# Kernel optimization log

Measured on AMD Instinct MI355X. Metric: run time of the kernel, lower is better.

Reference implementation:

```python
import jax, jax.numpy as jnp
import numpy as np

H = 2048      # hidden_size
K = 1024      # bottleneck_size
R = 3         # number of roles
B = 8         # batch
S = 2048      # sequence length
LN_EPS = 1e-5


def setup_inputs() -> dict:
    key = jax.random.key(0)
    ks = jax.random.split(key, 8)
    # torch nn.Linear default init ~ U(-1/sqrt(fan_in), 1/sqrt(fan_in)); scale similarly
    sd_d = 1.0 / np.sqrt(H)
    sd_u = 1.0 / np.sqrt(K)
    return {
        "role": jax.random.randint(ks[0], (B,), 0, R),
        "hidden_states": jax.random.normal(ks[1], (B, S, H), dtype=jnp.float32),
        # stacked per-role adapter params
        "W_down": jax.random.uniform(ks[2], (R, H, K), jnp.float32, -sd_d, sd_d),
        "b_down": jax.random.uniform(ks[3], (R, K), jnp.float32, -sd_d, sd_d),
        "W_up": jax.random.uniform(ks[4], (R, K, H), jnp.float32, -sd_u, sd_u),
        "b_up": jax.random.uniform(ks[5], (R, H), jnp.float32, -sd_u, sd_u),
        "gamma": jnp.ones((R, H), jnp.float32),
        "beta": jnp.zeros((R, H), jnp.float32),
    }


def reference(role, hidden_states, W_down, b_down, W_up, b_up, gamma, beta):
    # gather per-sample adapter params by role id: [B, H, K] etc.
    h = jnp.einsum("bsh,bhk->bsk", hidden_states, W_down[role]) + b_down[role][:, None, :]
    h = jax.nn.gelu(h, approximate=False)  # torch nn.GELU default = exact erf
    u = jnp.einsum("bsk,bkh->bsh", h, W_up[role]) + b_up[role][:, None, :]
    y = hidden_states + u
    # LayerNorm over last dim
    mean = jnp.mean(y, axis=-1, keepdims=True)
    var = jnp.mean(jnp.square(y - mean), axis=-1, keepdims=True)
    yn = (y - mean) * jax.lax.rsqrt(var + LN_EPS)
    return yn * gamma[role][:, None, :] + beta[role][:, None, :]
```

## Files before the change

### kernel.cpp

```cpp
#include <hip/hip_runtime.h>
#include <hip/hip_bf16.h>

#define H 2048
#define K 1024
#define R 3
#define BB 8
#define S 2048

typedef __bf16 bf16x8 __attribute__((ext_vector_type(8)));
typedef float f32x4 __attribute__((ext_vector_type(4)));
typedef unsigned short ushort8 __attribute__((ext_vector_type(8)));

static __device__ __forceinline__ unsigned short f2bf(float f) {
    unsigned int u = __float_as_uint(f);
    u += 0x7FFFu + ((u >> 16) & 1u);
    return (unsigned short)(u >> 16);
}

#define GLOAD_LDS16(g, l)                                                      \
    __builtin_amdgcn_global_load_lds(                                          \
        (const __attribute__((address_space(1))) void*)(g),                    \
        (__attribute__((address_space(3))) void*)(l), 16, 0, 0)

__global__ __launch_bounds__(256) void cvt_hs(const float* __restrict__ in,
                                              unsigned short* __restrict__ out,
                                              int n8) {
    int stride = gridDim.x * blockDim.x;
    for (int i = blockIdx.x * blockDim.x + threadIdx.x; i < n8; i += stride) {
        const float4* p = (const float4*)(in + (size_t)i * 8);
        float4 a = p[0], b = p[1];
        union { unsigned short us[8]; ushort8 v; } o;
        o.us[0] = f2bf(a.x); o.us[1] = f2bf(a.y);
        o.us[2] = f2bf(a.z); o.us[3] = f2bf(a.w);
        o.us[4] = f2bf(b.x); o.us[5] = f2bf(b.y);
        o.us[6] = f2bf(b.z); o.us[7] = f2bf(b.w);
        *(ushort8*)(out + (size_t)i * 8) = o.v;
    }
}

__global__ __launch_bounds__(256) void tpose(const float* __restrict__ in,
                                             unsigned short* __restrict__ out,
                                             int rows, int cols) {
    __shared__ float tile[32][33];
    int rr = blockIdx.z;
    const float* ip = in + (size_t)rr * rows * cols;
    unsigned short* op = out + (size_t)rr * rows * cols;
    int x = blockIdx.x * 32 + threadIdx.x;
    int y0 = blockIdx.y * 32 + threadIdx.y;
#pragma unroll
    for (int j = 0; j < 32; j += 8)
        tile[threadIdx.y + j][threadIdx.x] = ip[(size_t)(y0 + j) * cols + x];
    __syncthreads();
    int ox = blockIdx.y * 32 + threadIdx.x;
    int oy0 = blockIdx.x * 32 + threadIdx.y;
#pragma unroll
    for (int j = 0; j < 32; j += 8)
        op[(size_t)(oy0 + j) * rows + ox] = f2bf(tile[threadIdx.x][threadIdx.y + j]);
}

template <int KC, int EPI>
__global__ __launch_bounds__(512, 2) void gemm_8ph(
    const unsigned short* __restrict__ A, const unsigned short* __restrict__ Bt,
    const int* __restrict__ role, const float* __restrict__ bias,
    const unsigned short* __restrict__ resid, void* __restrict__ Out,
    float2* __restrict__ Part, int N) {
    constexpr int NT = KC / 64;
    __shared__ char smem[163840];
    const int tid = threadIdx.x;
    const int wid = tid >> 6, lane = tid & 63;
    const int wm = wid >> 2, wn = wid & 3;
    const int lr = lane & 15, lc = lane >> 4;

    const int nx = N >> 8;
    const int cpx = gridDim.x >> 3;
    const int orig = (blockIdx.x & 7) * cpx + (blockIdx.x >> 3);
    const int tn = orig % nx;
    const int tmz = orig / nx;
    const int tm = tmz & 7;
    const int z = tmz >> 3;
    const int r = role[z];

    const char* Ab = (const char*)(A + ((size_t)z * S + (size_t)tm * 256) * KC);
    const char* Bb = (const char*)(Bt + ((size_t)r * N + (size_t)tn * 256) * KC);

    const int P16 = tid * 16;

#define STAGE16(gbase, ldsbase, kt, half)                                      \
    do {                                                                       \
        _Pragma("unroll") for (int c_ = 0; c_ < 2; c_++) {                     \
            int P_ = c_ * 8192 + P16;                                          \
            int L_ = P_ ^ (((P_ >> 7) & 7) << 4);                              \
            const char* g_ = (gbase) +                                         \
                (size_t)((half) * 128 + (L_ >> 7)) * (KC * 2) +                \
                (size_t)(kt) * 128 + (L_ & 127);                               \
            GLOAD_LDS16(g_, (ldsbase) + (half) * 16384 + P_);                  \
        }                                                                      \
    } while (0)

    STAGE16(Ab, smem, 0, 0);            STAGE16(Ab, smem, 0, 1);
    STAGE16(Bb, smem + 98304, 0, 0);    STAGE16(Bb, smem + 98304, 0, 1);
    STAGE16(Ab, smem + 32768, 1, 0);    STAGE16(Ab, smem + 32768, 1, 1);
    STAGE16(Bb, smem + 131072, 1, 0);   STAGE16(Bb, smem + 131072, 1, 1);
    asm volatile("s_waitcnt vmcnt(8)" ::: "memory");
    __builtin_amdgcn_s_barrier();

    f32x4 acc[8][4] = {};
    const int swz = (lr & 7) << 4;
    const int ck0 = (lc << 4) ^ swz;
    const int ck1 = ck0 ^ 0x40;
    const char* sm = smem;

#define LDA4(ibase, base_)                                                     \
    _Pragma("unroll") for (int i_ = 0; i_ < 4; i_++) {                         \
        int rb_ = (wm * 128 + ((ibase) + i_) * 16 + lr) << 7;                  \
        a[i_][0] = *(const bf16x8*)(sm + (base_) + rb_ + ck0);                 \
        a[i_][1] = *(const bf16x8*)(sm + (base_) + rb_ + ck1); }
#define LDB2(jbase, base_)                                                     \
    _Pragma("unroll") for (int j_ = 0; j_ < 2; j_++) {                         \
        int rb_ = (wn * 64 + ((jbase) + j_) * 16 + lr) << 7;                   \
        b[(jbase) + j_][0] = *(const bf16x8*)(sm + 98304 + (base_) + rb_ + ck0); \
        b[(jbase) + j_][1] = *(const bf16x8*)(sm + 98304 + (base_) + rb_ + ck1); }
#define MFMA16(IOFF, JOFF)                                                     \
    _Pragma("unroll") for (int kk = 0; kk < 2; kk++)                           \
    _Pragma("unroll") for (int i_ = 0; i_ < 4; i_++)                           \
    _Pragma("unroll") for (int j_ = 0; j_ < 2; j_++)                           \
        acc[(IOFF) + i_][(JOFF) + j_] = __builtin_amdgcn_mfma_f32_16x16x32_bf16( \
            a[i_][kk], b[(JOFF) + j_][kk], acc[(IOFF) + i_][(JOFF) + j_], 0, 0, 0);
#define PH_MID()                                                               \
    __builtin_amdgcn_s_barrier();                                              \
    asm volatile("s_waitcnt lgkmcnt(0)" ::: "memory");                         \
    __builtin_amdgcn_s_setprio(1);
#define PH_END()                                                               \
    __builtin_amdgcn_s_setprio(0);                                             \
    __builtin_amdgcn_s_barrier();

    int as0 = 0, as1 = 1, as2 = 2;
#pragma unroll 1
    for (int t = 0; t < NT; t += 2) {
        bf16x8 a[4][2], b[4][2];
        const bool pf = (t + 2) < NT;
        const int saT = as0 * 32768, saT1 = as1 * 32768;
        char* stA2 = smem + as2 * 32768;
        char* stA3 = smem + as0 * 32768;
        LDA4(0, saT); LDB2(0, 0);
        if (pf) STAGE16(Ab, stA2, t + 2, 0);
        asm volatile("s_waitcnt lgkmcnt(8)" ::: "memory");
        PH_MID(); MFMA16(0, 0); PH_END();
        LDB2(2, 0);
        if (pf) STAGE16(Ab, stA2, t + 2, 1);
        PH_MID(); MFMA16(0, 2); PH_END();
        LDA4(4, saT);
        if (pf) STAGE16(Bb, smem + 98304, t + 2, 0);
        PH_MID(); MFMA16(4, 0); PH_END();
        if (pf) STAGE16(Bb, smem + 98304, t + 2, 1);
        PH_MID(); MFMA16(4, 2);
        __builtin_amdgcn_s_setprio(0);
        if (pf) asm volatile("s_waitcnt vmcnt(8)" ::: "memory");
        else    asm volatile("s_waitcnt vmcnt(0)" ::: "memory");
        __builtin_amdgcn_s_barrier();
        LDA4(0, saT1); LDB2(0, 32768);
        if (pf) STAGE16(Ab, stA3, t + 3, 0);
        asm volatile("s_waitcnt lgkmcnt(8)" ::: "memory");
        PH_MID(); MFMA16(0, 0); PH_END();
        LDB2(2, 32768);
        if (pf) STAGE16(Ab, stA3, t + 3, 1);
        PH_MID(); MFMA16(0, 2); PH_END();
        LDA4(4, saT1);
        if (pf) STAGE16(Bb, smem + 131072, t + 3, 0);
        PH_MID(); MFMA16(4, 0); PH_END();
        if (pf) STAGE16(Bb, smem + 131072, t + 3, 1);
        PH_MID(); MFMA16(4, 2);
        __builtin_amdgcn_s_setprio(0);
        if (pf) {
            asm volatile("s_waitcnt vmcnt(8)" ::: "memory");
            __builtin_amdgcn_s_barrier();
        }
        int t0 = as0; as0 = as2; as2 = as1; as1 = t0;
    }
#undef STAGE16
#undef LDA4
#undef LDB2
#undef MFMA16
#undef PH_MID
#undef PH_END

    const int base_m = tm * 256 + wm * 128;
    const int base_n = tn * 256 + wn * 64;
    float bn[4];
    const float* bp = bias + (size_t)r * N + base_n;
#pragma unroll
    for (int j = 0; j < 4; j++) bn[j] = bp[j * 16 + lr];

    if (EPI == 0) {
        unsigned short* o = (unsigned short*)Out;
#pragma unroll
        for (int i = 0; i < 8; i++) {
#pragma unroll
            for (int j = 0; j < 4; j++) {
#pragma unroll
                for (int q = 0; q < 4; q++) {
                    size_t grow = (size_t)z * S + base_m + i * 16 + lc * 4 + q;
                    int col = base_n + j * 16 + lr;
                    float x = acc[i][j][q] + bn[j];
                    float g = 0.5f * x * (1.0f + erff(x * 0.70710678118654752f));
                    o[grow * N + col] = f2bf(g);
                }
            }
        }
    } else {
        unsigned short* o = (unsigned short*)Out;
        float* pl = (float*)smem;
        __syncthreads();
#pragma unroll
        for (int i = 0; i < 8; i++) {
#pragma unroll
            for (int q = 0; q < 4; q++) {
                size_t grow = (size_t)z * S + base_m + i * 16 + lc * 4 + q;
                float s = 0.f, sq = 0.f;
#pragma unroll
                for (int j = 0; j < 4; j++) {
                    int col = base_n + j * 16 + lr;
                    float rv = __uint_as_float(((unsigned)resid[grow * (size_t)N + col]) << 16);
                    float y = acc[i][j][q] + bn[j] + rv;
                    o[grow * (size_t)N + col] = f2bf(y);
                    s += y; sq += y * y;
                }
#pragma unroll
                for (int off = 1; off < 16; off <<= 1) {
                    s  += __shfl_xor(s, off);
                    sq += __shfl_xor(sq, off);
                }
                if (lr == 0) {
                    int rloc = wm * 128 + i * 16 + lc * 4 + q;
                    pl[wn * 256 + rloc] = s;
                    pl[(4 + wn) * 256 + rloc] = sq;
                }
            }
        }
        __syncthreads();
        if (tid < 256) {
            float s  = pl[tid] + pl[256 + tid] + pl[512 + tid] + pl[768 + tid];
            float sq = pl[1024 + tid] + pl[1280 + tid] + pl[1536 + tid] + pl[1792 + tid];
            size_t grow = (size_t)z * S + tm * 256 + tid;
            Part[(size_t)tn * (BB * S) + grow] = make_float2(s, sq);
        }
    }
}

__global__ __launch_bounds__(256) void ln2(const unsigned short* __restrict__ ybf,
                                           const float2* __restrict__ part,
                                           const int* __restrict__ role,
                                           const float* __restrict__ gamma,
                                           const float* __restrict__ beta,
                                           float* __restrict__ out) {
    int row = blockIdx.x;
    int z = row >> 11;
    int r = role[z];
    float s = 0.f, ss = 0.f;
#pragma unroll
    for (int nb = 0; nb < 8; nb++) {
        float2 p = part[(size_t)nb * (BB * S) + row];
        s += p.x; ss += p.y;
    }
    float mean = s * (1.0f / H);
    float var = ss * (1.0f / H) - mean * mean;
    float rstd = rsqrtf(var + 1e-5f);
    int t = threadIdx.x;
    ushort8 yv = ((const ushort8*)(ybf + (size_t)row * H))[t];
    const float4* gp = (const float4*)(gamma + (size_t)r * H);
    const float4* bp = (const float4*)(beta + (size_t)r * H);
    float4 g0 = gp[2 * t], g1 = gp[2 * t + 1];
    float4 b0 = bp[2 * t], b1 = bp[2 * t + 1];
    float yo[8];
#pragma unroll
    for (int e = 0; e < 8; e++)
        yo[e] = (__uint_as_float(((unsigned)yv[e]) << 16) - mean) * rstd;
    float4 r0, r1;
    r0.x = yo[0] * g0.x + b0.x; r0.y = yo[1] * g0.y + b0.y;
    r0.z = yo[2] * g0.z + b0.z; r0.w = yo[3] * g0.w + b0.w;
    r1.x = yo[4] * g1.x + b1.x; r1.y = yo[5] * g1.y + b1.y;
    r1.z = yo[6] * g1.z + b1.z; r1.w = yo[7] * g1.w + b1.w;
    float4* op = (float4*)(out + (size_t)row * H);
    op[2 * t] = r0;
    op[2 * t + 1] = r1;
}

extern "C" void kernel_launch(void* const* d_in, const int* in_sizes, int n_in,
                              void* d_out, int out_size, void* d_ws, size_t ws_size,
                              hipStream_t stream) {
    const int* role = (const int*)d_in[0];
    const float* hs = (const float*)d_in[1];
    const float* Wd = (const float*)d_in[2];
    const float* bd = (const float*)d_in[3];
    const float* Wu = (const float*)d_in[4];
    const float* bu = (const float*)d_in[5];
    const float* gamma = (const float*)d_in[6];
    const float* beta = (const float*)d_in[7];
    float* out = (float*)d_out;

    char* ws = (char*)d_ws;
    unsigned short* hs_bf = (unsigned short*)ws;
    unsigned short* y_bf = (unsigned short*)ws;
    unsigned short* wd_t = (unsigned short*)(ws + 67108864);
    float2* part = (float2*)(ws + 67108864);
    unsigned short* wu_t = (unsigned short*)(ws + 67108864 + 12582912);
    unsigned short* h_ws = (unsigned short*)(ws + 67108864 + 2 * 12582912);

    cvt_hs<<<4096, 256, 0, stream>>>(hs, hs_bf, (BB * S * H) / 8);
    dim3 tb(32, 8);
    tpose<<<dim3(K / 32, H / 32, R), tb, 0, stream>>>(Wd, wd_t, H, K);
    tpose<<<dim3(H / 32, K / 32, R), tb, 0, stream>>>(Wu, wu_t, K, H);
    gemm_8ph<H, 0><<<(K / 256) * 8 * BB, 512, 0, stream>>>(hs_bf, wd_t, role, bd,
                                                           nullptr, h_ws, nullptr, K);
    gemm_8ph<K, 1><<<(H / 256) * 8 * BB, 512, 0, stream>>>(h_ws, wu_t, role, bu,
                                                           hs_bf, y_bf, part, H);
    ln2<<<BB * S, 256, 0, stream>>>(y_bf, part, role, gamma, beta, out);
}
```

Before: 256.6 us.

## Shrink GEMM LDS to 128KB with a two-buffer A pipeline

Replaces the triple-buffered A tile rotation (160KB LDS) with a fixed two-buffer layout for A and B (128KB). A for tile t+1 is now staged during compute of tile t instead of two tiles ahead, and the vmcnt waits are adjusted to match. The aim is lower LDS use, which may let more blocks fit per CU, in exchange for a shorter prefetch distance and more exposed load latency on A.

```diff
diff --git a/kernel.cpp b/kernel.cpp
--- a/kernel.cpp
+++ b/kernel.cpp
@@ -65,7 +65,7 @@
     const unsigned short* __restrict__ resid, void* __restrict__ Out,
     float2* __restrict__ Part, int N) {
     constexpr int NT = KC / 64;
-    __shared__ char smem[163840];
+    __shared__ char smem[131072];
     const int tid = threadIdx.x;
     const int wid = tid >> 6, lane = tid & 63;
     const int wm = wid >> 2, wn = wid & 3;
@@ -85,7 +85,7 @@
 
     const int P16 = tid * 16;
 
-#define STAGE16(gbase, ldsbase, kt, half)                                      \
+#define STAGE16(gbase, ldsoff, kt, half)                                       \
     do {                                                                       \
         _Pragma("unroll") for (int c_ = 0; c_ < 2; c_++) {                     \
             int P_ = c_ * 8192 + P16;                                          \
@@ -93,15 +93,14 @@
             const char* g_ = (gbase) +                                         \
                 (size_t)((half) * 128 + (L_ >> 7)) * (KC * 2) +                \
                 (size_t)(kt) * 128 + (L_ & 127);                               \
-            GLOAD_LDS16(g_, (ldsbase) + (half) * 16384 + P_);                  \
+            GLOAD_LDS16(g_, smem + (ldsoff) + (half) * 16384 + P_);            \
         }                                                                      \
     } while (0)
 
-    STAGE16(Ab, smem, 0, 0);            STAGE16(Ab, smem, 0, 1);
-    STAGE16(Bb, smem + 98304, 0, 0);    STAGE16(Bb, smem + 98304, 0, 1);
-    STAGE16(Ab, smem + 32768, 1, 0);    STAGE16(Ab, smem + 32768, 1, 1);
-    STAGE16(Bb, smem + 131072, 1, 0);   STAGE16(Bb, smem + 131072, 1, 1);
-    asm volatile("s_waitcnt vmcnt(8)" ::: "memory");
+    STAGE16(Ab, 0, 0, 0);        STAGE16(Ab, 0, 0, 1);
+    STAGE16(Bb, 32768, 0, 0);    STAGE16(Bb, 32768, 0, 1);
+    STAGE16(Bb, 98304, 1, 0);    STAGE16(Bb, 98304, 1, 1);
+    asm volatile("s_waitcnt vmcnt(4)" ::: "memory");
     __builtin_amdgcn_s_barrier();
 
     f32x4 acc[8][4] = {};
@@ -110,16 +109,16 @@
     const int ck1 = ck0 ^ 0x40;
     const char* sm = smem;
 
-#define LDA4(ibase, base_)                                                     \
+#define LDA4(ibase, SL)                                                        \
     _Pragma("unroll") for (int i_ = 0; i_ < 4; i_++) {                         \
         int rb_ = (wm * 128 + ((ibase) + i_) * 16 + lr) << 7;                  \
-        a[i_][0] = *(const bf16x8*)(sm + (base_) + rb_ + ck0);                 \
-        a[i_][1] = *(const bf16x8*)(sm + (base_) + rb_ + ck1); }
-#define LDB2(jbase, base_)                                                     \
+        a[i_][0] = *(const bf16x8*)(sm + (SL) + rb_ + ck0);                    \
+        a[i_][1] = *(const bf16x8*)(sm + (SL) + rb_ + ck1); }
+#define LDB2(jbase, SL)                                                        \
     _Pragma("unroll") for (int j_ = 0; j_ < 2; j_++) {                         \
         int rb_ = (wn * 64 + ((jbase) + j_) * 16 + lr) << 7;                   \
-        b[(jbase) + j_][0] = *(const bf16x8*)(sm + 98304 + (base_) + rb_ + ck0); \
-        b[(jbase) + j_][1] = *(const bf16x8*)(sm + 98304 + (base_) + rb_ + ck1); }
+        b[(jbase) + j_][0] = *(const bf16x8*)(sm + (SL) + 32768 + rb_ + ck0);  \
+        b[(jbase) + j_][1] = *(const bf16x8*)(sm + (SL) + 32768 + rb_ + ck1); }
 #define MFMA16(IOFF, JOFF)                                                     \
     _Pragma("unroll") for (int kk = 0; kk < 2; kk++)                           \
     _Pragma("unroll") for (int i_ = 0; i_ < 4; i_++)                           \
@@ -134,48 +133,44 @@
     __builtin_amdgcn_s_setprio(0);                                             \
     __builtin_amdgcn_s_barrier();
 
-    int as0 = 0, as1 = 1, as2 = 2;
 #pragma unroll 1
     for (int t = 0; t < NT; t += 2) {
         bf16x8 a[4][2], b[4][2];
-        const bool pf = (t + 2) < NT;
-        const int saT = as0 * 32768, saT1 = as1 * 32768;
-        char* stA2 = smem + as2 * 32768;
-        char* stA3 = smem + as0 * 32768;
-        LDA4(0, saT); LDB2(0, 0);
-        if (pf) STAGE16(Ab, stA2, t + 2, 0);
+        const bool pf2 = (t + 2) < NT, pf3 = (t + 3) < NT;
+        LDA4(0, 0); LDB2(0, 0);
+        STAGE16(Ab, 65536, t + 1, 0);
         asm volatile("s_waitcnt lgkmcnt(8)" ::: "memory");
         PH_MID(); MFMA16(0, 0); PH_END();
         LDB2(2, 0);
-        if (pf) STAGE16(Ab, stA2, t + 2, 1);
+        STAGE16(Ab, 65536, t + 1, 1);
         PH_MID(); MFMA16(0, 2); PH_END();
-        LDA4(4, saT);
-        if (pf) STAGE16(Bb, smem + 98304, t + 2, 0);
+        LDA4(4, 0);
+        if (pf2) STAGE16(Bb, 32768, t + 2, 0);
         PH_MID(); MFMA16(4, 0); PH_END();
-        if (pf) STAGE16(Bb, smem + 98304, t + 2, 1);
+        if (pf2) STAGE16(Bb, 32768, t + 2, 1);
         PH_MID(); MFMA16(4, 2);
         __builtin_amdgcn_s_setprio(0);
-        if (pf) asm volatile("s_waitcnt vmcnt(8)" ::: "memory");
-        else    asm volatile("s_waitcnt vmcnt(0)" ::: "memory");
+        if (pf2) asm volatile("s_waitcnt vmcnt(4)" ::: "memory");
+        else     asm volatile("s_waitcnt vmcnt(0)" ::: "memory");
         __builtin_amdgcn_s_barrier();
-        LDA4(0, saT1); LDB2(0, 32768);
-        if (pf) STAGE16(Ab, stA3, t + 3, 0);
+        LDA4(0, 65536); LDB2(0, 65536);
+        if (pf2) STAGE16(Ab, 0, t + 2, 0);
         asm volatile("s_waitcnt lgkmcnt(8)" ::: "memory");
         PH_MID(); MFMA16(0, 0); PH_END();
-        LDB2(2, 32768);
-        if (pf) STAGE16(Ab, stA3, t + 3, 1);
+        LDB2(2, 65536);
+        if (pf2) STAGE16(Ab, 0, t + 2, 1);
         PH_MID(); MFMA16(0, 2); PH_END();
-        LDA4(4, saT1);
-        if (pf) STAGE16(Bb, smem + 131072, t + 3, 0);
+        LDA4(4, 65536);
+        if (pf3) STAGE16(Bb, 98304, t + 3, 0);
         PH_MID(); MFMA16(4, 0); PH_END();
-        if (pf) STAGE16(Bb, smem + 131072, t + 3, 1);
+        if (pf3) STAGE16(Bb, 98304, t + 3, 1);
         PH_MID(); MFMA16(4, 2);
         __builtin_amdgcn_s_setprio(0);
-        if (pf) {
-            asm volatile("s_waitcnt vmcnt(8)" ::: "memory");
+        if (pf2) {
+            if (pf3) asm volatile("s_waitcnt vmcnt(4)" ::: "memory");
+            else     asm volatile("s_waitcnt vmcnt(0)" ::: "memory");
             __builtin_amdgcn_s_barrier();
         }
-        int t0 = as0; as0 = as2; as2 = as1; as1 = t0;
     }
 #undef STAGE16
 #undef LDA4
```

New measurement: 256.0 us. Within noise of the previous version (-0.2%).
